# Performance work log

Measured on AMD Instinct MI355X. Metric: run time of the kernel, lower is better.

Reference implementation:

```python
import jax, jax.numpy as jnp
import numpy as np

N_NODES = 100000
N_EDGES = 1600000
N_GRAPHS = 2048
DIM_IN, DIM_H, DIM_FC, DIM_OUT = 128, 128, 256, 8


def _glorot(key, shape):
    fan_in, fan_out = shape[0], shape[1]
    lim = float(np.sqrt(6.0 / (fan_in + fan_out)))
    return jax.random.uniform(key, shape, jnp.float32, -lim, lim)


def setup_inputs() -> dict:
    key = jax.random.key(0)
    ks = jax.random.split(key, 16)
    x = jax.random.normal(ks[0], (N_NODES, DIM_IN), jnp.float32)
    edge_index = jax.random.randint(ks[1], (2, N_EDGES), 0, N_NODES, jnp.int64)
    batch = jnp.sort(jax.random.randint(ks[2], (N_NODES,), 0, N_GRAPHS, jnp.int64))
    inp = {"x": x, "edge_index": edge_index, "batch": batch}
    # GraphConv layers: W_rel [in,out], W_root [in,out], b [out]
    dims = [(DIM_IN, DIM_H), (DIM_H, DIM_H), (DIM_H, DIM_H), (DIM_H, DIM_H)]
    for i, (di, do) in enumerate(dims, start=1):
        inp[f"W{i}_rel"] = _glorot(ks[2 + 3 * i], (di, do))
        inp[f"W{i}_root"] = _glorot(ks[3 + 3 * i], (di, do))
        inp[f"b{i}"] = jnp.zeros((do,), jnp.float32)
    inp["fc_w"] = _glorot(ks[3], (DIM_H, DIM_FC))
    inp["fc_b"] = jnp.zeros((DIM_FC,), jnp.float32)
    inp["reg_w"] = _glorot(ks[4], (DIM_FC, DIM_OUT))
    inp["reg_b"] = jnp.zeros((DIM_OUT,), jnp.float32)
    return inp


def _graph_conv(x, src, dst, w_rel, w_root, b):
    # PyG GraphConv (aggr='add'): out_i = W_rel @ sum_{j->i} x_j + W_root @ x_i + b
    agg = jax.ops.segment_sum(x[src], dst, num_segments=N_NODES)  # [N, d_in]
    return agg @ w_rel + x @ w_root + b


def reference(x, edge_index, batch,
              W1_rel, W1_root, b1, W2_rel, W2_root, b2,
              W3_rel, W3_root, b3, W4_rel, W4_root, b4,
              fc_w, fc_b, reg_w, reg_b):
    src, dst = edge_index[0], edge_index[1]
    h = jax.nn.relu(_graph_conv(x, src, dst, W1_rel, W1_root, b1))
    h = jax.nn.relu(_graph_conv(h, src, dst, W2_rel, W2_root, b2))
    h = jax.nn.relu(_graph_conv(h, src, dst, W3_rel, W3_root, b3))
    h = jax.nn.relu(_graph_conv(h, src, dst, W4_rel, W4_root, b4))
    # global_mean_pool over graphs
    sums = jax.ops.segment_sum(h, batch, num_segments=N_GRAPHS)  # [G, d]
    cnt = jax.ops.segment_sum(jnp.ones((h.shape[0],), h.dtype), batch,
                              num_segments=N_GRAPHS)
    pooled = sums / jnp.maximum(cnt, 1.0)[:, None]
    # dropout is identity at inference
    hfc = pooled @ fc_w + fc_b
    return hfc @ reg_w + reg_b  # [G, dim_out]
```

## Files before the change

### kernel.cpp

```cpp
#include <hip/hip_runtime.h>

#define N_NODES 100000
#define N_EDGES 1600000
#define N_GRAPHS 2048
#define DIM 128

#define NBUK 196
#define BUKSH 9
#define NCH 256
#define EPB 6250
#define NMAT (NBUK * NCH)

typedef short short8v __attribute__((ext_vector_type(8)));
typedef float float4v __attribute__((ext_vector_type(4)));

__device__ __forceinline__ unsigned short f2bf(float f) {
  union { float f; unsigned u; } x; x.f = f;
  unsigned r = x.u + 0x7fffu + ((x.u >> 16) & 1u);
  return (unsigned short)(r >> 16);
}
__device__ __forceinline__ float bfhi2f(unsigned bits) {
  union { unsigned u; float f; } x; x.u = bits; return x.f;
}
__device__ __forceinline__ void accum8(float* p, uint4 v) {
  p[0] += bfhi2f(v.x << 16); p[1] += bfhi2f(v.x & 0xffff0000u);
  p[2] += bfhi2f(v.y << 16); p[3] += bfhi2f(v.y & 0xffff0000u);
  p[4] += bfhi2f(v.z << 16); p[5] += bfhi2f(v.z & 0xffff0000u);
  p[6] += bfhi2f(v.w << 16); p[7] += bfhi2f(v.w & 0xffff0000u);
}

__global__ __launch_bounds__(256) void k_bcount(const int* __restrict__ dst, int* __restrict__ cntmat) {
  __shared__ int cnt[NBUK];
  int b = blockIdx.x, t = threadIdx.x;
  if (t < NBUK) cnt[t] = 0;
  __syncthreads();
  int e0 = b * EPB;
  for (int j = t; j < EPB; j += 256) atomicAdd(&cnt[dst[e0 + j] >> BUKSH], 1);
  __syncthreads();
  if (t < NBUK) cntmat[t * NCH + b] = cnt[t];
}

__global__ __launch_bounds__(256) void k_scan1g(const int* __restrict__ in, int n,
                                                int* __restrict__ tmp, int* __restrict__ bsum) {
  __shared__ int sh[256];
  int b = blockIdx.x, t = threadIdx.x;
  int base = b * 1024 + t * 4;
  int v[4], s = 0;
#pragma unroll
  for (int i = 0; i < 4; i++) { v[i] = (base + i < n) ? in[base + i] : 0; s += v[i]; }
  sh[t] = s;
  __syncthreads();
  for (int off = 1; off < 256; off <<= 1) {
    int x = (t >= off) ? sh[t - off] : 0;
    __syncthreads();
    sh[t] += x;
    __syncthreads();
  }
  int run = sh[t] - s;
#pragma unroll
  for (int i = 0; i < 4; i++) { run += v[i]; if (base + i < n) tmp[base + i] = run; }
  if (t == 255) bsum[b] = sh[255];
}

__global__ void k_scan2g(int* __restrict__ bsum, int nb) {
  __shared__ int sh[128];
  int t = threadIdx.x;
  int v = (t < nb) ? bsum[t] : 0;
  sh[t] = v;
  __syncthreads();
  for (int off = 1; off < 128; off <<= 1) {
    int x = (t >= off) ? sh[t - off] : 0;
    __syncthreads();
    sh[t] += x;
    __syncthreads();
  }
  if (t < nb) bsum[t] = sh[t] - v;
}

__global__ __launch_bounds__(256) void k_exc(const int* __restrict__ tmp, const int* __restrict__ bsum,
                                             const int* __restrict__ in, int n, int* __restrict__ outExc) {
  int i = blockIdx.x * 256 + threadIdx.x;
  if (i < n) outExc[i] = tmp[i] + bsum[i >> 10] - in[i];
}

__global__ __launch_bounds__(256) void k_bscatter(const int* __restrict__ src, const int* __restrict__ dst,
                                                  const int* __restrict__ base, int2* __restrict__ epk) {
  __shared__ int cur[NBUK];
  int b = blockIdx.x, t = threadIdx.x;
  if (t < NBUK) cur[t] = base[t * NCH + b];
  __syncthreads();
  int e0 = b * EPB;
  for (int j = t; j < EPB; j += 256) {
    int s = src[e0 + j], d = dst[e0 + j];
    int pos = atomicAdd(&cur[d >> BUKSH], 1);
    epk[pos] = make_int2(s, d);
  }
}

__global__ __launch_bounds__(256) void k_bfinish(const int2* __restrict__ epk, const int* __restrict__ base,
                                                 int* __restrict__ rowptr, int* __restrict__ col) {
  __shared__ int a[512];
  __shared__ int sh[256];
  int k = blockIdx.x, t = threadIdx.x;
  int bstart = base[k * NCH];
  int bend = (k + 1 < NBUK) ? base[(k + 1) * NCH] : N_EDGES;
  a[t] = 0; a[t + 256] = 0;
  __syncthreads();
  for (int i = bstart + t; i < bend; i += 256) atomicAdd(&a[epk[i].y - (k << BUKSH)], 1);
  __syncthreads();
  int c0 = a[2 * t], c1 = a[2 * t + 1];
  int s = c0 + c1;
  sh[t] = s;
  __syncthreads();
  for (int off = 1; off < 256; off <<= 1) {
    int x = (t >= off) ? sh[t - off] : 0;
    __syncthreads();
    sh[t] += x;
    __syncthreads();
  }
  int excl = sh[t] - s;
  int st0 = bstart + excl;
  int st1 = st0 + c0;
  int g0 = (k << BUKSH) + 2 * t, g1 = g0 + 1;
  if (g0 < N_NODES) rowptr[g0] = st0;
  if (g1 < N_NODES) rowptr[g1] = st1;
  if (k == NBUK - 1 && t == 0) rowptr[N_NODES] = N_EDGES;
  __syncthreads();
  a[2 * t] = st0; a[2 * t + 1] = st1;
  __syncthreads();
  for (int i = bstart + t; i < bend; i += 256) {
    int2 e = epk[i];
    int pos = atomicAdd(&a[e.y - (k << BUKSH)], 1);
    col[pos] = e.x;
  }
}

__global__ __launch_bounds__(256) void k_gptr(const int* __restrict__ batch, int* __restrict__ gptr) {
  int i = blockIdx.x * 256 + threadIdx.x;
  if (i >= N_NODES) return;
  int b = batch[i];
  int a = (i == 0) ? -1 : batch[i - 1];
  for (int g = a + 1; g <= b; g++) gptr[g] = i;
  if (i == N_NODES - 1) {
    for (int g = b + 1; g <= N_GRAPHS; g++) gptr[g] = N_NODES;
  }
}

__global__ __launch_bounds__(256) void k_cvtx(const float* __restrict__ x, unsigned short* __restrict__ h) {
  int i = blockIdx.x * 256 + threadIdx.x;
  if (i < N_NODES * DIM / 4) {
    float4 v = ((const float4*)x)[i];
    unsigned lo = (unsigned)f2bf(v.x) | ((unsigned)f2bf(v.y) << 16);
    unsigned hi = (unsigned)f2bf(v.z) | ((unsigned)f2bf(v.w) << 16);
    ((uint2*)h)[i] = make_uint2(lo, hi);
  }
}

__global__ __launch_bounds__(256) void k_cvtw(const float* w0, const float* w1, const float* w2, const float* w3,
                                              const float* w4, const float* w5, const float* w6, const float* w7,
                                              unsigned short* __restrict__ wbF) {
  int i = blockIdx.x * 256 + threadIdx.x;
  if (i < 4 * 8 * 8 * 64 * 8) {
    int j = i & 7, l = (i >> 3) & 63, c = (i >> 9) & 7, kc = (i >> 12) & 7, layer = i >> 15;
    int m = layer * 2 + (kc >> 2);
    const float* w;
    switch (m) {
      case 0: w = w0; break; case 1: w = w1; break; case 2: w = w2; break; case 3: w = w3; break;
      case 4: w = w4; break; case 5: w = w5; break; case 6: w = w6; break; default: w = w7; break;
    }
    int kin = (kc & 3) * 32 + ((l >> 4) * 8) + j;
    int n = c * 16 + (l & 15);
    wbF[i] = f2bf(w[kin * 128 + n]);
  }
}

__global__ __launch_bounds__(256) void k_agg(const int* __restrict__ rowptr, const int* __restrict__ col,
                                             const unsigned short* __restrict__ hIn,
                                             unsigned short* __restrict__ aggOut) {
  int node = blockIdx.x * 4 + (threadIdx.x >> 6);
  if (node >= N_NODES) return;
  int lane = threadIdx.x & 63;
  int sub = lane >> 4;
  int li = lane & 15;
  int s0 = rowptr[node], s1 = rowptr[node + 1];
  float p[8];
#pragma unroll
  for (int j = 0; j < 8; j++) p[j] = 0.f;

  int e = s0;
  for (; e + 16 <= s1; e += 16) {
    int c0 = col[e + sub];
    int c1 = col[e + 4 + sub];
    int c2 = col[e + 8 + sub];
    int c3 = col[e + 12 + sub];
    uint4 v0 = *(const uint4*)(hIn + (size_t)c0 * DIM + li * 8);
    uint4 v1 = *(const uint4*)(hIn + (size_t)c1 * DIM + li * 8);
    uint4 v2 = *(const uint4*)(hIn + (size_t)c2 * DIM + li * 8);
    uint4 v3 = *(const uint4*)(hIn + (size_t)c3 * DIM + li * 8);
    accum8(p, v0);
    accum8(p, v1);
    accum8(p, v2);
    accum8(p, v3);
  }
  if (e + 8 <= s1) {
    int c0 = col[e + sub];
    int c1 = col[e + 4 + sub];
    uint4 v0 = *(const uint4*)(hIn + (size_t)c0 * DIM + li * 8);
    uint4 v1 = *(const uint4*)(hIn + (size_t)c1 * DIM + li * 8);
    accum8(p, v0);
    accum8(p, v1);
    e += 8;
  }
  if (e + 4 <= s1) {
    int c0 = col[e + sub];
    uint4 v0 = *(const uint4*)(hIn + (size_t)c0 * DIM + li * 8);
    accum8(p, v0);
    e += 4;
  }
  if (e + sub < s1) {
    int c0 = col[e + sub];
    uint4 v0 = *(const uint4*)(hIn + (size_t)c0 * DIM + li * 8);
    accum8(p, v0);
  }

#pragma unroll
  for (int j = 0; j < 8; j++) {
    p[j] += __shfl_xor(p[j], 16, 64);
    p[j] += __shfl_xor(p[j], 32, 64);
  }

  if (sub == 0) {
    uint4 o;
    o.x = (unsigned)f2bf(p[0]) | ((unsigned)f2bf(p[1]) << 16);
    o.y = (unsigned)f2bf(p[2]) | ((unsigned)f2bf(p[3]) << 16);
    o.z = (unsigned)f2bf(p[4]) | ((unsigned)f2bf(p[5]) << 16);
    o.w = (unsigned)f2bf(p[6]) | ((unsigned)f2bf(p[7]) << 16);
    *(uint4*)(aggOut + (size_t)node * DIM + li * 8) = o;
  }
}

__global__ __launch_bounds__(256) void k_conv(const unsigned short* __restrict__ aggB,
                                              const unsigned short* __restrict__ hIn,
                                              const unsigned short* __restrict__ wbF,
                                              const float* __restrict__ bias,
                                              unsigned short* __restrict__ hOut) {
  __shared__ uint4 As[4096];
  const int t = threadIdx.x;
  const int row0b = blockIdx.x * 128;

#pragma unroll
  for (int j = 0; j < 8; j++) {
    int r = j * 16 + (t >> 4);
    int c = t & 15;
    int rsrc = row0b + r; if (rsrc > N_NODES - 1) rsrc = N_NODES - 1;
    uint4 v = *(const uint4*)(aggB + (size_t)rsrc * DIM + c * 8);
    As[((r >> 4) * 32 + c) * 16 + ((r & 15) ^ c)] = v;
  }
#pragma unroll
  for (int j = 0; j < 8; j++) {
    int r = j * 16 + (t >> 4);
    int c = t & 15;
    int rsrc = row0b + r; if (rsrc > N_NODES - 1) rsrc = N_NODES - 1;
    uint4 v = *(const uint4*)(hIn + (size_t)rsrc * DIM + c * 8);
    As[((r >> 4) * 32 + 16 + c) * 16 + ((r & 15) ^ c)] = v;
  }
  __syncthreads();

  const int wave = t >> 6, lane = t & 63;
  const int row0 = row0b + wave * 32;

  float4v acc[2][8];
#pragma unroll
  for (int r = 0; r < 2; r++)
#pragma unroll
    for (int c = 0; c < 8; c++)
#pragma unroll
      for (int i = 0; i < 4; i++) acc[r][c][i] = 0.f;

#pragma unroll
  for (int kc = 0; kc < 8; kc++) {
    short8v afr[2];
#pragma unroll
    for (int r = 0; r < 2; r++) {
      int g = wave * 2 + r;
      int c = kc * 4 + (lane >> 4);
      int rr = (lane & 15) ^ (c & 15);
      afr[r] = *(const short8v*)&As[(g * 32 + c) * 16 + rr];
    }
#pragma unroll
    for (int c = 0; c < 8; c++) {
      short8v bfr = *(const short8v*)(wbF + (size_t)((kc * 8 + c) * 64 + lane) * 8);
#pragma unroll
      for (int r = 0; r < 2; r++)
        acc[r][c] = __builtin_amdgcn_mfma_f32_16x16x32_bf16(afr[r], bfr, acc[r][c], 0, 0, 0);
    }
  }

#pragma unroll
  for (int r = 0; r < 2; r++) {
    int rbase = row0 + r * 16 + (lane >> 4) * 4;
#pragma unroll
    for (int c = 0; c < 8; c++) {
      int colidx = c * 16 + (lane & 15);
      float bv = bias[colidx];
#pragma unroll
      for (int i = 0; i < 4; i++) {
        int row = rbase + i;
        if (row < N_NODES) {
          float v = acc[r][c][i] + bv;
          v = v > 0.f ? v : 0.f;
          hOut[row * DIM + colidx] = f2bf(v);
        }
      }
    }
  }
}

__global__ __launch_bounds__(256) void k_pool(const unsigned short* __restrict__ h,
                                              const int* __restrict__ gptr,
                                              float* __restrict__ pooledMean) {
  int g = blockIdx.x * 4 + (threadIdx.x >> 6);
  if (g >= N_GRAPHS) return;
  int lane = threadIdx.x & 63;
  int li = lane & 15;
  int s0 = gptr[g], s1 = gptr[g + 1];
  float p[8];
#pragma unroll
  for (int j = 0; j < 8; j++) p[j] = 0.f;
  int f1 = s1 * 16;
  for (int f = s0 * 16 + lane; f < f1; f += 64) {
    uint4 v = ((const uint4*)h)[f];
    accum8(p, v);
  }
#pragma unroll
  for (int j = 0; j < 8; j++) {
    p[j] += __shfl_xor(p[j], 16, 64);
    p[j] += __shfl_xor(p[j], 32, 64);
  }
  float inv = (s1 > s0) ? 1.f / (float)(s1 - s0) : 0.f;
  if (lane < 16) {
    float4 o0 = make_float4(p[0] * inv, p[1] * inv, p[2] * inv, p[3] * inv);
    float4 o1 = make_float4(p[4] * inv, p[5] * inv, p[6] * inv, p[7] * inv);
    *(float4*)(pooledMean + g * DIM + li * 8) = o0;
    *(float4*)(pooledMean + g * DIM + li * 8 + 4) = o1;
  }
}

__global__ __launch_bounds__(256) void k_fc(const float* __restrict__ pooledMean,
                                            const float* __restrict__ fc_w, const float* __restrict__ fc_b,
                                            const float* __restrict__ reg_w, const float* __restrict__ reg_b,
                                            float* __restrict__ out) {
  __shared__ float sp[128];
  __shared__ float shfc[256];
  __shared__ float red[64];
  int g = blockIdx.x, t = threadIdx.x;
  if (t < 128) sp[t] = pooledMean[g * DIM + t];
  __syncthreads();
  float a = fc_b[t];
  for (int k = 0; k < 128; k++) a += sp[k] * fc_w[k * 256 + t];
  shfc[t] = a;
  __syncthreads();
  if (t < 64) {
    int o = t & 7, seg = t >> 3;
    float r = 0.f;
    for (int j = seg * 32; j < seg * 32 + 32; j++) r += shfc[j] * reg_w[j * 8 + o];
    red[t] = r;
  }
  __syncthreads();
  if (t < 8) {
    float r = reg_b[t];
    for (int s = 0; s < 8; s++) r += red[s * 8 + t];
    out[g * 8 + t] = r;
  }
}

extern "C" void kernel_launch(void* const* d_in, const int* in_sizes, int n_in,
                              void* d_out, int out_size, void* d_ws, size_t ws_size,
                              hipStream_t stream) {
  (void)in_sizes; (void)n_in; (void)out_size; (void)ws_size;
  const float* x = (const float*)d_in[0];
  const int* ei = (const int*)d_in[1];
  const int* src = ei;
  const int* dst = ei + N_EDGES;
  const int* batch = (const int*)d_in[2];
  const float* Wrel[4]  = {(const float*)d_in[3], (const float*)d_in[6], (const float*)d_in[9],  (const float*)d_in[12]};
  const float* Wroot[4] = {(const float*)d_in[4], (const float*)d_in[7], (const float*)d_in[10], (const float*)d_in[13]};
  const float* bias[4]  = {(const float*)d_in[5], (const float*)d_in[8], (const float*)d_in[11], (const float*)d_in[14]};
  const float* fc_w  = (const float*)d_in[15];
  const float* fc_b  = (const float*)d_in[16];
  const float* reg_w = (const float*)d_in[17];
  const float* reg_b = (const float*)d_in[18];
  float* out = (float*)d_out;

  char* ws = (char*)d_ws;
  size_t off = 0;
  auto alloc = [&](size_t b) -> char* {
    char* p = ws + off;
    off = (off + b + 255) & ~(size_t)255;
    return p;
  };
  int* rowptr = (int*)alloc((N_NODES + 1) * 4);
  int* cntmat = (int*)alloc((size_t)NMAT * 4);
  int* tmpB   = (int*)alloc((size_t)NMAT * 4);
  int* bsumB  = (int*)alloc(64 * 4);
  int* base   = (int*)alloc((size_t)NMAT * 4);
  int2* epk   = (int2*)alloc((size_t)N_EDGES * 8);
  int* colws  = (int*)alloc((size_t)N_EDGES * 4);
  int* gptr   = (int*)alloc((N_GRAPHS + 1) * 4);
  unsigned short* wbF = (unsigned short*)alloc((size_t)4 * 32768 * 2);
  unsigned short* h_a = (unsigned short*)alloc((size_t)N_NODES * DIM * 2);
  unsigned short* h_b = (unsigned short*)alloc((size_t)N_NODES * DIM * 2);
  unsigned short* agg = (unsigned short*)alloc((size_t)N_NODES * DIM * 2);
  float* pooled = (float*)alloc((size_t)N_GRAPHS * DIM * 4);

  k_bcount<<<NCH, 256, 0, stream>>>(dst, cntmat);
  k_scan1g<<<NMAT / 1024, 256, 0, stream>>>(cntmat, NMAT, tmpB, bsumB);
  k_scan2g<<<1, 128, 0, stream>>>(bsumB, NMAT / 1024);
  k_exc<<<(NMAT + 255) / 256, 256, 0, stream>>>(tmpB, bsumB, cntmat, NMAT, base);
  k_bscatter<<<NCH, 256, 0, stream>>>(src, dst, base, epk);
  k_bfinish<<<NBUK, 256, 0, stream>>>(epk, base, rowptr, colws);

  k_gptr<<<(N_NODES + 255) / 256, 256, 0, stream>>>(batch, gptr);
  k_cvtx<<<(N_NODES * DIM / 4 + 255) / 256, 256, 0, stream>>>(x, h_a);
  k_cvtw<<<(4 * 32768 + 255) / 256, 256, 0, stream>>>(
      Wrel[0], Wroot[0], Wrel[1], Wroot[1], Wrel[2], Wroot[2], Wrel[3], Wroot[3], wbF);

  unsigned short* h_in = h_a;
  unsigned short* h_out = h_b;
  for (int l = 0; l < 4; l++) {
    k_agg<<<(N_NODES + 3) / 4, 256, 0, stream>>>(rowptr, colws, h_in, agg);
    k_conv<<<(N_NODES + 127) / 128, 256, 0, stream>>>(
        agg, h_in, wbF + (size_t)l * 32768, bias[l], h_out);
    unsigned short* t2 = h_in; h_in = h_out; h_out = t2;
  }

  k_pool<<<(N_GRAPHS + 3) / 4, 256, 0, stream>>>(h_in, gptr, pooled);
  k_fc<<<N_GRAPHS, 256, 0, stream>>>(pooled, fc_w, fc_b, reg_w, reg_b, out);
}
```

Measured before the change: 583.3 us.

## Sort nodes by degree for aggregation wave balance and pack fp32 accumulation

Builds a degree-sorted node permutation through a counting sort (per-block degree histograms, a scan, then a scatter), so each aggregation block processes nodes with similar in-degree and its wavefronts diverge less. The aggregation accumulator is also switched to two-wide float vectors so the compiler can issue packed fp32 adds. In exchange it adds five small preprocessing launches and an indirection through the order array, and output rows are written in scattered rather than sequential order.

```diff
diff --git a/kernel.cpp b/kernel.cpp
--- a/kernel.cpp
+++ b/kernel.cpp
@@ -11,8 +11,13 @@
 #define EPB 6250
 #define NMAT (NBUK * NCH)
 
+#define NDB 98
+#define DBINS 64
+#define DMAT (DBINS * NDB)
+
 typedef short short8v __attribute__((ext_vector_type(8)));
 typedef float float4v __attribute__((ext_vector_type(4)));
+typedef float float2v __attribute__((ext_vector_type(2)));
 
 __device__ __forceinline__ unsigned short f2bf(float f) {
   union { float f; unsigned u; } x; x.f = f;
@@ -27,6 +32,13 @@
   p[2] += bfhi2f(v.y << 16); p[3] += bfhi2f(v.y & 0xffff0000u);
   p[4] += bfhi2f(v.z << 16); p[5] += bfhi2f(v.z & 0xffff0000u);
   p[6] += bfhi2f(v.w << 16); p[7] += bfhi2f(v.w & 0xffff0000u);
+}
+__device__ __forceinline__ void accum8pk(float2v* p, uint4 v) {
+  float2v t;
+  t[0] = bfhi2f(v.x << 16); t[1] = bfhi2f(v.x & 0xffff0000u); p[0] += t;
+  t[0] = bfhi2f(v.y << 16); t[1] = bfhi2f(v.y & 0xffff0000u); p[1] += t;
+  t[0] = bfhi2f(v.z << 16); t[1] = bfhi2f(v.z & 0xffff0000u); p[2] += t;
+  t[0] = bfhi2f(v.w << 16); t[1] = bfhi2f(v.w & 0xffff0000u); p[3] += t;
 }
 
 __global__ __launch_bounds__(256) void k_bcount(const int* __restrict__ dst, int* __restrict__ cntmat) {
@@ -132,6 +144,40 @@
     int2 e = epk[i];
     int pos = atomicAdd(&a[e.y - (k << BUKSH)], 1);
     col[pos] = e.x;
+  }
+}
+
+__global__ __launch_bounds__(256) void k_dcnt(const int* __restrict__ rowptr, int* __restrict__ dcnt) {
+  __shared__ int h[DBINS];
+  int b = blockIdx.x, t = threadIdx.x;
+  if (t < DBINS) h[t] = 0;
+  __syncthreads();
+  int base = b * 1024;
+  for (int j = t; j < 1024; j += 256) {
+    int n = base + j;
+    if (n < N_NODES) {
+      int d = rowptr[n + 1] - rowptr[n];
+      atomicAdd(&h[d > 63 ? 63 : d], 1);
+    }
+  }
+  __syncthreads();
+  if (t < DBINS) dcnt[t * NDB + b] = h[t];
+}
+
+__global__ __launch_bounds__(256) void k_dscatter(const int* __restrict__ rowptr,
+                                                  const int* __restrict__ dbase, int* __restrict__ order) {
+  __shared__ int cur[DBINS];
+  int b = blockIdx.x, t = threadIdx.x;
+  if (t < DBINS) cur[t] = dbase[t * NDB + b];
+  __syncthreads();
+  int base = b * 1024;
+  for (int j = t; j < 1024; j += 256) {
+    int n = base + j;
+    if (n < N_NODES) {
+      int d = rowptr[n + 1] - rowptr[n];
+      int pos = atomicAdd(&cur[d > 63 ? 63 : d], 1);
+      order[pos] = n;
+    }
   }
 }
 
@@ -174,18 +220,20 @@
   }
 }
 
-__global__ __launch_bounds__(256) void k_agg(const int* __restrict__ rowptr, const int* __restrict__ col,
+__global__ __launch_bounds__(256) void k_agg(const int* __restrict__ order, const int* __restrict__ rowptr,
+                                             const int* __restrict__ col,
                                              const unsigned short* __restrict__ hIn,
                                              unsigned short* __restrict__ aggOut) {
-  int node = blockIdx.x * 4 + (threadIdx.x >> 6);
-  if (node >= N_NODES) return;
+  int widx = blockIdx.x * 4 + (threadIdx.x >> 6);
+  if (widx >= N_NODES) return;
+  int node = order[widx];
   int lane = threadIdx.x & 63;
   int sub = lane >> 4;
   int li = lane & 15;
   int s0 = rowptr[node], s1 = rowptr[node + 1];
-  float p[8];
-#pragma unroll
-  for (int j = 0; j < 8; j++) p[j] = 0.f;
+  float2v p[4];
+#pragma unroll
+  for (int j = 0; j < 4; j++) { p[j][0] = 0.f; p[j][1] = 0.f; }
 
   int e = s0;
   for (; e + 16 <= s1; e += 16) {
@@ -197,44 +245,47 @@
     uint4 v1 = *(const uint4*)(hIn + (size_t)c1 * DIM + li * 8);
     uint4 v2 = *(const uint4*)(hIn + (size_t)c2 * DIM + li * 8);
     uint4 v3 = *(const uint4*)(hIn + (size_t)c3 * DIM + li * 8);
-    accum8(p, v0);
-    accum8(p, v1);
-    accum8(p, v2);
-    accum8(p, v3);
+    accum8pk(p, v0);
+    accum8pk(p, v1);
+    accum8pk(p, v2);
+    accum8pk(p, v3);
   }
   if (e + 8 <= s1) {
     int c0 = col[e + sub];
     int c1 = col[e + 4 + sub];
     uint4 v0 = *(const uint4*)(hIn + (size_t)c0 * DIM + li * 8);
     uint4 v1 = *(const uint4*)(hIn + (size_t)c1 * DIM + li * 8);
-    accum8(p, v0);
-    accum8(p, v1);
+    accum8pk(p, v0);
+    accum8pk(p, v1);
     e += 8;
   }
   if (e + 4 <= s1) {
     int c0 = col[e + sub];
     uint4 v0 = *(const uint4*)(hIn + (size_t)c0 * DIM + li * 8);
-    accum8(p, v0);
+    accum8pk(p, v0);
     e += 4;
   }
   if (e + sub < s1) {
     int c0 = col[e + sub];
     uint4 v0 = *(const uint4*)(hIn + (size_t)c0 * DIM + li * 8);
-    accum8(p, v0);
-  }
-
-#pragma unroll
-  for (int j = 0; j < 8; j++) {
-    p[j] += __shfl_xor(p[j], 16, 64);
-    p[j] += __shfl_xor(p[j], 32, 64);
+    accum8pk(p, v0);
+  }
+
+#pragma unroll
+  for (int j = 0; j < 4; j++) {
+#pragma unroll
+    for (int q = 0; q < 2; q++) {
+      p[j][q] += __shfl_xor(p[j][q], 16, 64);
+      p[j][q] += __shfl_xor(p[j][q], 32, 64);
+    }
   }
 
   if (sub == 0) {
     uint4 o;
-    o.x = (unsigned)f2bf(p[0]) | ((unsigned)f2bf(p[1]) << 16);
-    o.y = (unsigned)f2bf(p[2]) | ((unsigned)f2bf(p[3]) << 16);
-    o.z = (unsigned)f2bf(p[4]) | ((unsigned)f2bf(p[5]) << 16);
-    o.w = (unsigned)f2bf(p[6]) | ((unsigned)f2bf(p[7]) << 16);
+    o.x = (unsigned)f2bf(p[0][0]) | ((unsigned)f2bf(p[0][1]) << 16);
+    o.y = (unsigned)f2bf(p[1][0]) | ((unsigned)f2bf(p[1][1]) << 16);
+    o.z = (unsigned)f2bf(p[2][0]) | ((unsigned)f2bf(p[2][1]) << 16);
+    o.w = (unsigned)f2bf(p[3][0]) | ((unsigned)f2bf(p[3][1]) << 16);
     *(uint4*)(aggOut + (size_t)node * DIM + li * 8) = o;
   }
 }
@@ -402,10 +453,15 @@
   int* rowptr = (int*)alloc((N_NODES + 1) * 4);
   int* cntmat = (int*)alloc((size_t)NMAT * 4);
   int* tmpB   = (int*)alloc((size_t)NMAT * 4);
-  int* bsumB  = (int*)alloc(64 * 4);
+  int* bsumB  = (int*)alloc(128 * 4);
   int* base   = (int*)alloc((size_t)NMAT * 4);
   int2* epk   = (int2*)alloc((size_t)N_EDGES * 8);
   int* colws  = (int*)alloc((size_t)N_EDGES * 4);
+  int* dcnt   = (int*)alloc((size_t)DMAT * 4);
+  int* dtmp   = (int*)alloc((size_t)DMAT * 4);
+  int* dbsum  = (int*)alloc(128 * 4);
+  int* dbase  = (int*)alloc((size_t)DMAT * 4);
+  int* order  = (int*)alloc((size_t)N_NODES * 4);
   int* gptr   = (int*)alloc((N_GRAPHS + 1) * 4);
   unsigned short* wbF = (unsigned short*)alloc((size_t)4 * 32768 * 2);
   unsigned short* h_a = (unsigned short*)alloc((size_t)N_NODES * DIM * 2);
@@ -420,6 +476,12 @@
   k_bscatter<<<NCH, 256, 0, stream>>>(src, dst, base, epk);
   k_bfinish<<<NBUK, 256, 0, stream>>>(epk, base, rowptr, colws);
 
+  k_dcnt<<<NDB, 256, 0, stream>>>(rowptr, dcnt);
+  k_scan1g<<<(DMAT + 1023) / 1024, 256, 0, stream>>>(dcnt, DMAT, dtmp, dbsum);
+  k_scan2g<<<1, 128, 0, stream>>>(dbsum, (DMAT + 1023) / 1024);
+  k_exc<<<(DMAT + 255) / 256, 256, 0, stream>>>(dtmp, dbsum, dcnt, DMAT, dbase);
+  k_dscatter<<<NDB, 256, 0, stream>>>(rowptr, dbase, order);
+
   k_gptr<<<(N_NODES + 255) / 256, 256, 0, stream>>>(batch, gptr);
   k_cvtx<<<(N_NODES * DIM / 4 + 255) / 256, 256, 0, stream>>>(x, h_a);
   k_cvtw<<<(4 * 32768 + 255) / 256, 256, 0, stream>>>(
@@ -428,7 +490,7 @@
   unsigned short* h_in = h_a;
   unsigned short* h_out = h_b;
   for (int l = 0; l < 4; l++) {
-    k_agg<<<(N_NODES + 3) / 4, 256, 0, stream>>>(rowptr, colws, h_in, agg);
+    k_agg<<<(N_NODES + 3) / 4, 256, 0, stream>>>(order, rowptr, colws, h_in, agg);
     k_conv<<<(N_NODES + 127) / 128, 256, 0, stream>>>(
         agg, h_in, wbF + (size_t)l * 32768, bias[l], h_out);
     unsigned short* t2 = h_in; h_in = h_out; h_out = t2;
```

After: 608.3 us. +4.3%, slower.
